# Optimization experiments

Measured on AMD Instinct MI355X. Metric: run time of the kernel, lower is better.

Reference implementation:

```python
import jax, jax.numpy as jnp
import numpy as np

B, T, D_K, N_HEADS, D_FF, VOCAB, N_LAYERS = 4, 1024, 1024, 16, 4096, 65, 6


def setup_inputs() -> dict:
    key = jax.random.key(0)
    ks = jax.random.split(key, 12)
    f = lambda k, sh: jax.random.normal(k, sh, dtype=jnp.float32) * 0.02
    return {
        "batchData": jax.random.randint(ks[0], (B, T), 0, VOCAB),
        "target": jax.random.randint(ks[1], (B, T), 0, VOCAB),
        "pos": jnp.arange(T),
        "Wtok": f(ks[2], (VOCAB, D_K)),
        "Wpos": f(ks[3], (T, D_K)),
        "Wq": f(ks[4], (D_K, D_K)), "bq": jnp.zeros((D_K,), jnp.float32),
        "Wk": f(ks[5], (D_K, D_K)), "bk": jnp.zeros((D_K,), jnp.float32),
        "Wv": f(ks[6], (D_K, D_K)), "bv": jnp.zeros((D_K,), jnp.float32),
        "W1": f(ks[7], (D_K, D_FF)), "b1": jnp.zeros((D_FF,), jnp.float32),
        "W2": f(ks[8], (D_FF, D_K)), "b2": jnp.zeros((D_K,), jnp.float32),
        "ln_w": jnp.ones((D_K,), jnp.float32),
        "Wf": f(ks[9], (D_K, VOCAB)), "bf": jnp.zeros((VOCAB,), jnp.float32),
        "n_layers": N_LAYERS,
        "n_heads": N_HEADS,
    }


def layer_norm(x, w, eps=1e-5):
    m = jnp.mean(x, axis=-1, keepdims=True)
    v = jnp.var(x, axis=-1, keepdims=True)
    return (x - m) / jnp.sqrt(v + eps) * w


def reference(batchData, target, pos, Wtok, Wpos, Wq, bq, Wk, bk, Wv, bv,
              W1, b1, W2, b2, ln_w, Wf, bf, n_layers, n_heads):
    x = Wtok[batchData] + Wpos[pos]  # [B, T, C] (pos embedding broadcasts)
    Bsz, Tlen, C = x.shape
    dh = C // n_heads
    mask = jnp.tril(jnp.ones((Tlen, Tlen), dtype=bool))
    inv_sqrt_dk = 1.0 / jnp.sqrt(jnp.float32(C))  # source divides by sqrt(full d_k)

    def block(x):
        q = (x @ Wq + bq).reshape(Bsz, Tlen, n_heads, dh).transpose(0, 2, 1, 3)
        k = (x @ Wk + bk).reshape(Bsz, Tlen, n_heads, dh).transpose(0, 2, 1, 3)
        v = (x @ Wv + bv).reshape(Bsz, Tlen, n_heads, dh).transpose(0, 2, 1, 3)
        scores = jnp.einsum('bhqd,bhkd->bhqk', q, k) * inv_sqrt_dk
        scores = jnp.where(mask, scores, -jnp.inf)
        attn = jax.nn.softmax(scores, axis=-1)
        h = jnp.einsum('bhqk,bhkd->bhqd', attn, v)
        h = h.transpose(0, 2, 1, 3).reshape(Bsz, Tlen, C)
        h = h + layer_norm(h, ln_w)           # x = x + ln(x) (shared ln)
        ff = jax.nn.relu(h @ W1 + b1) @ W2 + b2
        return ff + layer_norm(ff, ln_w)      # same shared ln again

    # ModuleList repeats the SAME block object, so weights are shared across layers
    for _ in range(n_layers):
        x = block(x)

    logits = x @ Wf + bf                       # [B, T, V]
    probs = jax.nn.softmax(logits, axis=1)     # softmax over T, as in source
    pred = probs.reshape(Bsz * Tlen, -1)
    onehot = jax.nn.one_hot(target.reshape(-1), VOCAB, dtype=jnp.float32)
    # F.cross_entropy with soft (one-hot float) targets
    loss = -jnp.mean(jnp.sum(onehot * jax.nn.log_softmax(pred, axis=-1), axis=-1))
    return loss, probs
```

## Files before the change

kernel.cpp:

```cpp
#include <hip/hip_runtime.h>

typedef __attribute__((ext_vector_type(8))) short bh8;
typedef __attribute__((ext_vector_type(4))) float f4v;

constexpr int VOC = 65;
constexpr int NL  = 6;
constexpr int Mrow = 4096;

__device__ inline float b2f(unsigned short u) {
  union { unsigned int i; float f; } x; x.i = ((unsigned int)u) << 16; return x.f;
}
__device__ inline unsigned short f2b(float f) {
  union { float f; unsigned int i; } x; x.f = f;
  return (unsigned short)((x.i + 0x7FFFu + ((x.i >> 16) & 1u)) >> 16);
}
__device__ inline void gld16(const void* g, void* l) {
  __builtin_amdgcn_global_load_lds(
      (const __attribute__((address_space(1))) unsigned int*)g,
      (__attribute__((address_space(3))) unsigned int*)l, 16, 0, 0);
}
__device__ inline bh8 lds_swz(const unsigned short* base, int row, int colbyte) {
  int off = row * 128 + (colbyte ^ ((row & 7) << 4));
  return *(const bh8*)((const char*)base + off);
}
__device__ inline f4v mfma16(bh8 a, bh8 b, f4v c) {
  return __builtin_amdgcn_mfma_f32_16x16x32_bf16(a, b, c, 0, 0, 0);
}
#define WAITV(n) asm volatile("s_waitcnt vmcnt(" #n ")" ::: "memory")
#define LGKM0 asm volatile("s_waitcnt lgkmcnt(0)" ::: "memory")
#define LGKM8 asm volatile("s_waitcnt lgkmcnt(8)" ::: "memory")
#define SBAR0 __builtin_amdgcn_sched_barrier(0)
#define BAR __builtin_amdgcn_s_barrier()

__global__ __launch_bounds__(256) void wt_conv(const float* __restrict__ src,
    unsigned short* __restrict__ dst, int K, int N) {
  __shared__ float t[32][33];
  int k0 = blockIdx.x * 32, n0 = blockIdx.y * 32;
  int tid = threadIdx.x;
#pragma unroll
  for (int i = 0; i < 4; ++i) {
    int idx = tid + i * 256;
    int kr = idx >> 5, nc = idx & 31;
    t[kr][nc] = (n0 + nc < N) ? src[(size_t)(k0 + kr) * N + n0 + nc] : 0.f;
  }
  __syncthreads();
#pragma unroll
  for (int i = 0; i < 4; ++i) {
    int idx = tid + i * 256;
    int nr = idx >> 5, kc = idx & 31;
    dst[(size_t)(n0 + nr) * K + k0 + kc] = f2b(t[kc][nr]);
  }
}

__global__ __launch_bounds__(256) void bias_prep(
    const float* __restrict__ bq, const float* __restrict__ bk,
    const float* __restrict__ bv, const float* __restrict__ bf,
    float* __restrict__ bqkv, float* __restrict__ bfp) {
  int i = blockIdx.x * 256 + threadIdx.x;
  if (i < 1024) bqkv[i] = bq[i];
  else if (i < 2048) bqkv[i] = bk[i - 1024];
  else if (i < 3072) bqkv[i] = bv[i - 2048];
  else if (i < 3200) bfp[i - 3072] = (i - 3072 < VOC) ? bf[i - 3072] : 0.f;
}

__global__ __launch_bounds__(256) void embed_bf(const int* __restrict__ tok,
    const float* __restrict__ Wtok, const float* __restrict__ Wpos,
    unsigned short* __restrict__ Xb) {
  int bt = blockIdx.x, t = bt & 1023, tid = threadIdx.x;
  int id = tok[bt];
  float4 a = ((const float4*)(Wtok + (size_t)id * 1024))[tid];
  float4 p = ((const float4*)(Wpos + (size_t)t * 1024))[tid];
  ushort4 o;
  o.x = f2b(a.x + p.x); o.y = f2b(a.y + p.y);
  o.z = f2b(a.z + p.z); o.w = f2b(a.w + p.w);
  ((ushort4*)(Xb + (size_t)bt * 1024))[tid] = o;
}

template <bool RELU, bool PART, bool VT>
__global__ __launch_bounds__(512, 1) void gemm256(
    const unsigned short* __restrict__ A, const unsigned short* __restrict__ Bt,
    const float* __restrict__ bias, void* __restrict__ Cout,
    unsigned short* __restrict__ Vtout, long N, long Kloop, long lda, long ldb,
    int MT, int NT, int CM, int CN) {
  __shared__ unsigned short Abuf[2][256 * 64];
  __shared__ unsigned short Bbuf[2][256 * 64];
  const int tid = threadIdx.x, lane = tid & 63, w = tid >> 6;
  const int wr = w >> 2, wc = w & 3;
  const int lr = lane & 15, lh = lane >> 4, lh4 = lh * 4;

  const int x = (int)blockIdx.x & 7, j = (int)blockIdx.x >> 3;
  const int gM = MT / CM;
  const int rowT = (x % gM) * CM + (j % CM);
  const int c = (x / gM) * CN + (j / CM);
  const int colT = c % NT, ksl = c / NT;
  const long row0 = (long)rowT * 256, col0 = (long)colT * 256;
  const long kOff = (long)ksl * Kloop;

  f4v acc[8][4];
#pragma unroll
  for (int i = 0; i < 8; ++i)
#pragma unroll
    for (int jj = 0; jj < 4; ++jj) acc[i][jj] = f4v{0.f, 0.f, 0.f, 0.f};

  const int rg = tid >> 3, sIdx = tid & 7;
  const int ch = sIdx ^ (rg & 7);
  const unsigned short* Ap = A + (row0 + rg) * lda + kOff + ch * 8;
  const unsigned short* Bp = Bt + (col0 + rg) * ldb + kOff + ch * 8;

  auto stA = [&](int t, int h) {
    const long k0 = (long)t << 6;
#pragma unroll
    for (int i = 0; i < 2; ++i)
      gld16(Ap + (long)(h * 128 + i * 64) * lda + k0,
            &Abuf[t & 1][(h * 128 + i * 64) * 64 + tid * 8]);
  };
  auto stB = [&](int t, int h) {
    const long k0 = (long)t << 6;
#pragma unroll
    for (int i = 0; i < 2; ++i)
      gld16(Bp + (long)(h * 128 + i * 64) * ldb + k0,
            &Bbuf[t & 1][(h * 128 + i * 64) * 64 + tid * 8]);
  };

  const int nt = (int)(Kloop >> 6);
  stA(0, 0); stA(0, 1); stB(0, 0); stB(0, 1);
  stA(1, 0); stA(1, 1); stB(1, 0);
  WAITV(6);
  BAR;

  const int sl0 = (lh ^ (lr & 7)) * 8;
  const int sl1 = ((4 + lh) ^ (lr & 7)) * 8;

  for (int t = 0; t < nt; ++t) {
    const unsigned short* Ab = Abuf[t & 1];
    const unsigned short* Bb = Bbuf[t & 1];
    bh8 a0[4][2], a1[4][2], b0[2][2], b1[2][2];
#pragma unroll
    for (int mi = 0; mi < 4; ++mi) {
      const int row = (2 * mi + wr) * 16 + lr;
      a0[mi][0] = *(const bh8*)&Ab[row * 64 + sl0];
      a0[mi][1] = *(const bh8*)&Ab[row * 64 + sl1];
    }
#pragma unroll
    for (int ni = 0; ni < 2; ++ni) {
      const int row = (4 * ni + wc) * 16 + lr;
      b0[ni][0] = *(const bh8*)&Bb[row * 64 + sl0];
      b0[ni][1] = *(const bh8*)&Bb[row * 64 + sl1];
    }
    if (t + 1 < nt) stB(t + 1, 1);
    LGKM8;
    BAR;
    LGKM0; SBAR0;
    __builtin_amdgcn_s_setprio(1);
#pragma unroll
    for (int mi = 0; mi < 4; ++mi)
#pragma unroll
      for (int ni = 0; ni < 2; ++ni) {
        acc[mi][ni] = mfma16(a0[mi][0], b0[ni][0], acc[mi][ni]);
        acc[mi][ni] = mfma16(a0[mi][1], b0[ni][1], acc[mi][ni]);
      }
    __builtin_amdgcn_s_setprio(0);
    BAR;
#pragma unroll
    for (int mi = 0; mi < 4; ++mi) {
      const int row = (2 * (mi + 4) + wr) * 16 + lr;
      a1[mi][0] = *(const bh8*)&Ab[row * 64 + sl0];
      a1[mi][1] = *(const bh8*)&Ab[row * 64 + sl1];
    }
    if (t + 2 < nt) stA(t + 2, 0);
    BAR;
    LGKM0; SBAR0;
    __builtin_amdgcn_s_setprio(1);
#pragma unroll
    for (int mi = 0; mi < 4; ++mi)
#pragma unroll
      for (int ni = 0; ni < 2; ++ni) {
        acc[mi + 4][ni] = mfma16(a1[mi][0], b0[ni][0], acc[mi + 4][ni]);
        acc[mi + 4][ni] = mfma16(a1[mi][1], b0[ni][1], acc[mi + 4][ni]);
      }
    __builtin_amdgcn_s_setprio(0);
    BAR;
#pragma unroll
    for (int ni = 0; ni < 2; ++ni) {
      const int row = (4 * (ni + 2) + wc) * 16 + lr;
      b1[ni][0] = *(const bh8*)&Bb[row * 64 + sl0];
      b1[ni][1] = *(const bh8*)&Bb[row * 64 + sl1];
    }
    if (t + 2 < nt) stA(t + 2, 1);
    BAR;
    LGKM0; SBAR0;
    __builtin_amdgcn_s_setprio(1);
#pragma unroll
    for (int mi = 0; mi < 4; ++mi)
#pragma unroll
      for (int ni = 0; ni < 2; ++ni) {
        acc[mi][ni + 2] = mfma16(a0[mi][0], b1[ni][0], acc[mi][ni + 2]);
        acc[mi][ni + 2] = mfma16(a0[mi][1], b1[ni][1], acc[mi][ni + 2]);
      }
    __builtin_amdgcn_s_setprio(0);
    BAR;
    if (t + 2 < nt) stB(t + 2, 0);
    BAR;
    SBAR0;
    __builtin_amdgcn_s_setprio(1);
#pragma unroll
    for (int mi = 0; mi < 4; ++mi)
#pragma unroll
      for (int ni = 0; ni < 2; ++ni) {
        acc[mi + 4][ni + 2] = mfma16(a1[mi][0], b1[ni][0], acc[mi + 4][ni + 2]);
        acc[mi + 4][ni + 2] = mfma16(a1[mi][1], b1[ni][1], acc[mi + 4][ni + 2]);
      }
    __builtin_amdgcn_s_setprio(0);
    if (t + 1 < nt) {
      if (t + 2 < nt) { WAITV(6); } else { WAITV(0); }
      BAR;
    }
  }

  if (PART) {
    unsigned short* P = (unsigned short*)Cout + (size_t)ksl * 4096 * 1024;
#pragma unroll
    for (int mi = 0; mi < 8; ++mi)
#pragma unroll
      for (int ni = 0; ni < 4; ++ni) {
        long col = col0 + (4 * ni + wc) * 16 + lr;
#pragma unroll
        for (int r = 0; r < 4; ++r) {
          long row = row0 + (2 * mi + wr) * 16 + lh4 + r;
          P[row * N + col] = f2b(acc[mi][ni][r]);
        }
      }
    return;
  }
  if (VT && col0 >= 2048) {
#pragma unroll
    for (int mi = 0; mi < 8; ++mi)
#pragma unroll
      for (int ni = 0; ni < 4; ++ni) {
        int col = (int)col0 + (4 * ni + wc) * 16 + lr;
        float bb = bias[col];
        int cc = col - 2048;
        long row = row0 + (2 * mi + wr) * 16 + lh4;
        int bi = (int)(row >> 10), tt = (int)(row & 1023);
        ushort4 o;
        o.x = f2b(acc[mi][ni][0] + bb);
        o.y = f2b(acc[mi][ni][1] + bb);
        o.z = f2b(acc[mi][ni][2] + bb);
        o.w = f2b(acc[mi][ni][3] + bb);
        *(ushort4*)&Vtout[((size_t)(bi * 16 + (cc >> 6)) * 64 + (cc & 63)) *
                              1024 + tt] = o;
      }
    return;
  }
#pragma unroll
  for (int mi = 0; mi < 8; ++mi)
#pragma unroll
    for (int ni = 0; ni < 4; ++ni) {
      long col = col0 + (4 * ni + wc) * 16 + lr;
      float bb = bias[col];
      const float qsc = (VT && col < 1024) ? 0.03125f : 1.0f;
#pragma unroll
      for (int r = 0; r < 4; ++r) {
        long row = row0 + (2 * mi + wr) * 16 + lh4 + r;
        float v = acc[mi][ni][r] + bb;
        if (VT) v *= qsc;
        if (RELU) v = fmaxf(v, 0.f);
        ((unsigned short*)Cout)[row * N + col] = f2b(v);
      }
    }
}

template <int TM, int TN, bool RELU, bool F32OUT>
__global__ __launch_bounds__(256) void gemm4(
    const unsigned short* __restrict__ A, const unsigned short* __restrict__ Bt,
    const float* __restrict__ bias, void* __restrict__ Cout, long N, long K) {
  constexpr int MI = TM / 32, NI = TN / 32;
  constexpr int ABUF = TM * 64, BBUF = TN * 64;
  __shared__ unsigned short As[2 * ABUF];
  __shared__ unsigned short Bs[2 * BBUF];
  const int tid = threadIdx.x;
  const int lane = tid & 63, w = tid >> 6;
  const int wr = w >> 1, wc = w & 1;
  const int lr = lane & 15, lh = lane >> 4, lh4 = lh * 4;
  const long row0 = (long)blockIdx.x * TM, col0 = (long)blockIdx.y * TN;
  f4v acc[MI][NI];
#pragma unroll
  for (int i = 0; i < MI; ++i)
#pragma unroll
    for (int j = 0; j < NI; ++j) acc[i][j] = f4v{0.f, 0.f, 0.f, 0.f};
  const int rg = tid >> 3, s = tid & 7;
  const int ch = s ^ (rg & 7);
  const unsigned short* Ap = A + (row0 + rg) * K + ch * 8;
  const unsigned short* Bp = Bt + (col0 + rg) * K + ch * 8;
  auto stage = [&](int t, int buf) {
    const long k0 = (long)t << 6;
#pragma unroll
    for (int i = 0; i < MI; ++i)
      gld16(Ap + i * 32 * K + k0, &As[buf * ABUF + (i * 256 + tid) * 8]);
#pragma unroll
    for (int i = 0; i < NI; ++i)
      gld16(Bp + i * 32 * K + k0, &Bs[buf * BBUF + (i * 256 + tid) * 8]);
  };
  const int nt = (int)(K >> 6);
  stage(0, 0);
  for (int t = 0; t < nt; ++t) {
    const int cur = t & 1;
    if (t + 1 < nt) {
      stage(t + 1, cur ^ 1);
      WAITV(6);
    } else {
      WAITV(0);
    }
    BAR;
    const unsigned short* Ab = &As[cur * ABUF];
    const unsigned short* Bb = &Bs[cur * BBUF];
#pragma unroll
    for (int ks = 0; ks < 2; ++ks) {
      bh8 a[MI], b[NI];
      const int slot = ((ks << 2) | lh) ^ (lr & 7);
#pragma unroll
      for (int mi = 0; mi < MI; ++mi) {
        int m = wr * (TM / 2) + mi * 16 + lr;
        a[mi] = *(const bh8*)((const char*)Ab + m * 128 + slot * 16);
      }
#pragma unroll
      for (int ni = 0; ni < NI; ++ni) {
        int n = wc * (TN / 2) + ni * 16 + lr;
        b[ni] = *(const bh8*)((const char*)Bb + n * 128 + slot * 16);
      }
#pragma unroll
      for (int mi = 0; mi < MI; ++mi)
#pragma unroll
        for (int ni = 0; ni < NI; ++ni)
          acc[mi][ni] = mfma16(a[mi], b[ni], acc[mi][ni]);
    }
    BAR;
  }
#pragma unroll
  for (int mi = 0; mi < MI; ++mi) {
#pragma unroll
    for (int ni = 0; ni < NI; ++ni) {
      long col = col0 + wc * (TN / 2) + ni * 16 + lr;
      float bb = bias[col];
#pragma unroll
      for (int r = 0; r < 4; ++r) {
        long row = row0 + wr * (TM / 2) + mi * 16 + lh4 + r;
        float v = acc[mi][ni][r] + bb;
        if (RELU) v = fmaxf(v, 0.f);
        if (F32OUT) ((float*)Cout)[row * N + col] = v;
        else ((unsigned short*)Cout)[row * N + col] = f2b(v);
      }
    }
  }
}

__global__ __launch_bounds__(256) void attn_mfma(
    const unsigned short* __restrict__ QKV, const unsigned short* __restrict__ Vt,
    unsigned short* __restrict__ Hout) {
  __shared__ unsigned short Ks[2][64 * 64];
  __shared__ unsigned short Vs[2][64 * 64];
  __shared__ unsigned short Ps[4][16 * 64];
  const int tid = threadIdx.x, w = tid >> 6, lane = tid & 63;
  const int wid = ((int)blockIdx.x & 7) * 128 + ((int)blockIdx.x >> 3);
  const int bh = wid >> 4;
  const int qt = 15 - (wid & 15);
  const int b = bh >> 4, h = bh & 15;
  const int lr = lane & 15, lh = lane >> 4, lh4 = lh * 4;

  const unsigned short* qp =
      QKV + (size_t)(b * 1024 + qt * 64 + w * 16 + lr) * 3072 + h * 64 + lh * 8;
  bh8 aq0 = *(const bh8*)qp;
  bh8 aq1 = *(const bh8*)(qp + 32);

  f4v o[4];
#pragma unroll
  for (int i = 0; i < 4; ++i) o[i] = f4v{0.f, 0.f, 0.f, 0.f};
  float m = -1e30f, l = 0.f;

  const int r8 = tid >> 3, slot = tid & 7;
  unsigned short* pw = &Ps[w][0];

  auto stage = [&](int kt, int buf) {
    int r = r8, c8 = (slot ^ (r & 7)) * 8;
    gld16(QKV + (size_t)(b * 1024 + kt * 64 + r) * 3072 + 1024 + h * 64 + c8,
          &Ks[buf][tid * 8]);
    gld16(Vt + (size_t)(bh * 64 + r) * 1024 + kt * 64 + c8, &Vs[buf][tid * 8]);
    r = r8 + 32; c8 = (slot ^ (r & 7)) * 8;
    gld16(QKV + (size_t)(b * 1024 + kt * 64 + r) * 3072 + 1024 + h * 64 + c8,
          &Ks[buf][2048 + tid * 8]);
    gld16(Vt + (size_t)(bh * 64 + r) * 1024 + kt * 64 + c8,
          &Vs[buf][2048 + tid * 8]);
  };

  stage(0, 0);

  for (int kt = 0; kt <= qt; ++kt) {
    const int cur = kt & 1;
    if (kt < qt) {
      stage(kt + 1, cur ^ 1);
      WAITV(4);
    } else {
      WAITV(0);
    }
    BAR;

    f4v s[4];
#pragma unroll
    for (int nt = 0; nt < 4; ++nt) {
      bh8 k0 = lds_swz(Ks[cur], nt * 16 + lr, lh * 16);
      bh8 k1 = lds_swz(Ks[cur], nt * 16 + lr, lh * 16 + 64);
      f4v z = f4v{0.f, 0.f, 0.f, 0.f};
      z = mfma16(k0, aq0, z);
      z = mfma16(k1, aq1, z);
      s[nt] = z;
    }
    const bool diag = (kt == qt);
    if (diag) {
      const int qloc = w * 16 + lr;
#pragma unroll
      for (int nt = 0; nt < 4; ++nt)
#pragma unroll
        for (int r = 0; r < 4; ++r)
          if ((nt * 16 + lh4 + r) > qloc) s[nt][r] = -1e30f;
    }
    float tm = fmaxf(fmaxf(fmaxf(s[0][0], s[0][1]), fmaxf(s[0][2], s[0][3])),
                     fmaxf(fmaxf(s[1][0], s[1][1]), fmaxf(s[1][2], s[1][3])));
    float tm2 = fmaxf(fmaxf(fmaxf(s[2][0], s[2][1]), fmaxf(s[2][2], s[2][3])),
                      fmaxf(fmaxf(s[3][0], s[3][1]), fmaxf(s[3][2], s[3][3])));
    tm = fmaxf(tm, tm2);
    tm = fmaxf(tm, __shfl_xor(tm, 16));
    tm = fmaxf(tm, __shfl_xor(tm, 32));

    const bool resc = __any(tm > m + 8.f);
    const float mu = resc ? fmaxf(m, tm) : m;
    float sum = 0.f;
#pragma unroll
    for (int nt = 0; nt < 4; ++nt)
#pragma unroll
      for (int r = 0; r < 4; ++r) {
        float e = __expf(s[nt][r] - mu);
        s[nt][r] = e;
        sum += e;
      }
    sum += __shfl_xor(sum, 16);
    sum += __shfl_xor(sum, 32);
    if (resc) {
      float corr = __expf(m - mu);
      m = mu;
      l = l * corr + sum;
      float c0 = __shfl(corr, lh4 + 0), c1 = __shfl(corr, lh4 + 1);
      float c2 = __shfl(corr, lh4 + 2), c3 = __shfl(corr, lh4 + 3);
#pragma unroll
      for (int nt = 0; nt < 4; ++nt) {
        o[nt][0] *= c0; o[nt][1] *= c1; o[nt][2] *= c2; o[nt][3] *= c3;
      }
    } else {
      l += sum;
    }
#pragma unroll
    for (int nt = 0; nt < 4; ++nt) {
      unsigned int u0, u1;
      asm("v_cvt_pk_bf16_f32 %0, %1, %2" : "=v"(u0) : "v"(s[nt][0]), "v"(s[nt][1]));
      asm("v_cvt_pk_bf16_f32 %0, %1, %2" : "=v"(u1) : "v"(s[nt][2]), "v"(s[nt][3]));
      uint2 pk{u0, u1};
      *(uint2*)((char*)pw + lr * 128 + ((nt * 32 + lh * 8) ^ ((lr & 7) << 4))) = pk;
    }
    bh8 pa0 = lds_swz(pw, lr, lh * 16);
    bh8 pa1 = lds_swz(pw, lr, lh * 16 + 64);
#pragma unroll
    for (int nt = 0; nt < 4; ++nt) {
      bh8 v0 = lds_swz(Vs[cur], nt * 16 + lr, lh * 16);
      bh8 v1 = lds_swz(Vs[cur], nt * 16 + lr, lh * 16 + 64);
      o[nt] = mfma16(pa0, v0, o[nt]);
      o[nt] = mfma16(pa1, v1, o[nt]);
    }
    BAR;
  }
  float linv = 1.f / l;
  float l0 = __shfl(linv, lh4 + 0), l1 = __shfl(linv, lh4 + 1);
  float l2 = __shfl(linv, lh4 + 2), l3 = __shfl(linv, lh4 + 3);
  const size_t rowb = (size_t)(b * 1024 + qt * 64 + w * 16);
#pragma unroll
  for (int nt = 0; nt < 4; ++nt) {
    int col = h * 64 + nt * 16 + lr;
    Hout[(rowb + lh4 + 0) * 1024 + col] = f2b(o[nt][0] * l0);
    Hout[(rowb + lh4 + 1) * 1024 + col] = f2b(o[nt][1] * l1);
    Hout[(rowb + lh4 + 2) * 1024 + col] = f2b(o[nt][2] * l2);
    Hout[(rowb + lh4 + 3) * 1024 + col] = f2b(o[nt][3] * l3);
  }
}

__global__ __launch_bounds__(256) void ln_res_bf(
    const unsigned short* __restrict__ Xi, const float* __restrict__ wln,
    unsigned short* __restrict__ Y) {
  int row = blockIdx.x, tid = threadIdx.x;
  ushort4 u = ((const ushort4*)(Xi + (size_t)row * 1024))[tid];
  float x0 = b2f(u.x), x1 = b2f(u.y), x2 = b2f(u.z), x3 = b2f(u.w);
  float s = x0 + x1 + x2 + x3;
  float ss = x0 * x0 + x1 * x1 + x2 * x2 + x3 * x3;
#pragma unroll
  for (int off = 32; off; off >>= 1) {
    s += __shfl_xor(s, off);
    ss += __shfl_xor(ss, off);
  }
  __shared__ float sw[4], ssw[4];
  int wv = tid >> 6, ln = tid & 63;
  if (ln == 0) { sw[wv] = s; ssw[wv] = ss; }
  __syncthreads();
  s = sw[0] + sw[1] + sw[2] + sw[3];
  ss = ssw[0] + ssw[1] + ssw[2] + ssw[3];
  float mean = s * (1.f / 1024.f);
  float var = ss * (1.f / 1024.f) - mean * mean;
  float rstd = rsqrtf(var + 1e-5f);
  float4 wv4 = ((const float4*)wln)[tid];
  ushort4 out;
  out.x = f2b(x0 + (x0 - mean) * rstd * wv4.x);
  out.y = f2b(x1 + (x1 - mean) * rstd * wv4.y);
  out.z = f2b(x2 + (x2 - mean) * rstd * wv4.z);
  out.w = f2b(x3 + (x3 - mean) * rstd * wv4.w);
  ((ushort4*)(Y + (size_t)row * 1024))[tid] = out;
}

__global__ __launch_bounds__(256) void ln2_fuse(
    const unsigned short* __restrict__ P, const float* __restrict__ b2,
    const float* __restrict__ wln, unsigned short* __restrict__ Y) {
  int row = blockIdx.x, tid = threadIdx.x;
  const size_t plane = (size_t)4096 * 1024;
  float x0 = 0.f, x1 = 0.f, x2 = 0.f, x3 = 0.f;
#pragma unroll
  for (int pl = 0; pl < 4; ++pl) {
    ushort4 u = *(const ushort4*)&P[pl * plane + (size_t)row * 1024 + tid * 4];
    x0 += b2f(u.x); x1 += b2f(u.y); x2 += b2f(u.z); x3 += b2f(u.w);
  }
  float4 bb = ((const float4*)b2)[tid];
  x0 += bb.x; x1 += bb.y; x2 += bb.z; x3 += bb.w;
  float s = x0 + x1 + x2 + x3;
  float ss = x0 * x0 + x1 * x1 + x2 * x2 + x3 * x3;
#pragma unroll
  for (int off = 32; off; off >>= 1) {
    s += __shfl_xor(s, off);
    ss += __shfl_xor(ss, off);
  }
  __shared__ float sw[4], ssw[4];
  int wv = tid >> 6, ln = tid & 63;
  if (ln == 0) { sw[wv] = s; ssw[wv] = ss; }
  __syncthreads();
  s = sw[0] + sw[1] + sw[2] + sw[3];
  ss = ssw[0] + ssw[1] + ssw[2] + ssw[3];
  float mean = s * (1.f / 1024.f);
  float var = ss * (1.f / 1024.f) - mean * mean;
  float rstd = rsqrtf(var + 1e-5f);
  float4 wv4 = ((const float4*)wln)[tid];
  ushort4 out;
  out.x = f2b(x0 + (x0 - mean) * rstd * wv4.x);
  out.y = f2b(x1 + (x1 - mean) * rstd * wv4.y);
  out.z = f2b(x2 + (x2 - mean) * rstd * wv4.z);
  out.w = f2b(x3 + (x3 - mean) * rstd * wv4.w);
  ((ushort4*)(Y + (size_t)row * 1024))[tid] = out;
}

__global__ __launch_bounds__(256) void softmaxT_kernel(
    const float* __restrict__ logits, float* __restrict__ probs) {
  int b = blockIdx.x / VOC;
  int v = blockIdx.x - b * VOC;
  const float* src = logits + (size_t)b * 1024 * 128 + v;
  float vals[4];
  float m = -1e30f;
#pragma unroll
  for (int i = 0; i < 4; ++i) {
    int t = threadIdx.x + 256 * i;
    vals[i] = src[(size_t)t * 128];
    m = fmaxf(m, vals[i]);
  }
#pragma unroll
  for (int off = 32; off; off >>= 1) m = fmaxf(m, __shfl_xor(m, off));
  __shared__ float sm[4], ssum[4];
  int wv = threadIdx.x >> 6, ln = threadIdx.x & 63;
  if (ln == 0) sm[wv] = m;
  __syncthreads();
  m = fmaxf(fmaxf(sm[0], sm[1]), fmaxf(sm[2], sm[3]));
  float s = 0.f;
#pragma unroll
  for (int i = 0; i < 4; ++i) { vals[i] = __expf(vals[i] - m); s += vals[i]; }
#pragma unroll
  for (int off = 32; off; off >>= 1) s += __shfl_xor(s, off);
  if (ln == 0) ssum[wv] = s;
  __syncthreads();
  s = ssum[0] + ssum[1] + ssum[2] + ssum[3];
  float inv = 1.f / s;
  float* dst = probs + (size_t)b * 1024 * VOC + v;
#pragma unroll
  for (int i = 0; i < 4; ++i) {
    int t = threadIdx.x + 256 * i;
    dst[(size_t)t * VOC] = vals[i] * inv;
  }
}

__global__ __launch_bounds__(256) void loss_rows_kernel(
    const float* __restrict__ probs, const int* __restrict__ tgt,
    float* __restrict__ partial) {
  int wv = threadIdx.x >> 6, lane = threadIdx.x & 63;
  int row = blockIdx.x * 4 + wv;
  const float* p = probs + (size_t)row * VOC;
  float x0 = p[lane];
  float x1 = (lane == 0) ? p[64] : -1e30f;
  float m = fmaxf(x0, x1);
#pragma unroll
  for (int off = 32; off; off >>= 1) m = fmaxf(m, __shfl_xor(m, off));
  float s = __expf(x0 - m) + ((lane == 0) ? __expf(x1 - m) : 0.f);
#pragma unroll
  for (int off = 32; off; off >>= 1) s += __shfl_xor(s, off);
  if (lane == 0) {
    int tg = tgt[row];
    partial[row] = (p[tg] - m) - logf(s);
  }
}

__global__ __launch_bounds__(256) void loss_final_kernel(
    const float* __restrict__ partial, float* __restrict__ out) {
  float s = 0.f;
  for (int i = threadIdx.x; i < Mrow; i += 256) s += partial[i];
#pragma unroll
  for (int off = 32; off; off >>= 1) s += __shfl_xor(s, off);
  __shared__ float sw[4];
  int wv = threadIdx.x >> 6, ln = threadIdx.x & 63;
  if (ln == 0) sw[wv] = s;
  __syncthreads();
  if (threadIdx.x == 0) out[0] = -(sw[0] + sw[1] + sw[2] + sw[3]) / (float)Mrow;
}

extern "C" void kernel_launch(void* const* d_in, const int* in_sizes, int n_in,
                              void* d_out, int out_size, void* d_ws,
                              size_t ws_size, hipStream_t stream) {
  (void)in_sizes; (void)n_in; (void)out_size; (void)ws_size;
  const int*   tok    = (const int*)d_in[0];
  const int*   target = (const int*)d_in[1];
  const float* Wtok   = (const float*)d_in[3];
  const float* Wpos   = (const float*)d_in[4];
  const float* Wq = (const float*)d_in[5];  const float* bq = (const float*)d_in[6];
  const float* Wk = (const float*)d_in[7];  const float* bk = (const float*)d_in[8];
  const float* Wv = (const float*)d_in[9];  const float* bv = (const float*)d_in[10];
  const float* W1 = (const float*)d_in[11]; const float* b1 = (const float*)d_in[12];
  const float* W2 = (const float*)d_in[13]; const float* b2 = (const float*)d_in[14];
  const float* lnw = (const float*)d_in[15];
  const float* Wf = (const float*)d_in[16]; const float* bf = (const float*)d_in[17];
  float* out = (float*)d_out;

  char* p = (char*)d_ws;
  unsigned short* Xb    = (unsigned short*)p; p += (size_t)Mrow * 1024 * 2;
  unsigned short* QKVb  = (unsigned short*)p; p += (size_t)Mrow * 3072 * 2;
  unsigned short* Vt    = (unsigned short*)p; p += (size_t)64 * 64 * 1024 * 2;
  unsigned short* Hb    = (unsigned short*)p; p += (size_t)Mrow * 1024 * 2;
  unsigned short* F2b   = (unsigned short*)p; p += (size_t)Mrow * 1024 * 2;
  unsigned short* FF1b  = (unsigned short*)p; p += (size_t)Mrow * 4096 * 2;
  unsigned short* WqkvT = (unsigned short*)p; p += (size_t)3072 * 1024 * 2;
  unsigned short* W1T   = (unsigned short*)p; p += (size_t)4096 * 1024 * 2;
  unsigned short* W2T   = (unsigned short*)p; p += (size_t)1024 * 4096 * 2;
  unsigned short* WfT   = (unsigned short*)p; p += (size_t)128 * 1024 * 2;
  float* bqkv = (float*)p; p += 3072 * 4;
  float* bfp  = (float*)p; p += 128 * 4;
  float* LOG  = (float*)p; p += (size_t)Mrow * 128 * 4;
  float* PART = (float*)p; p += Mrow * 4;
  unsigned short* Pff2 = QKVb;

  wt_conv<<<dim3(32, 32), 256, 0, stream>>>(Wq, WqkvT,                1024, 1024);
  wt_conv<<<dim3(32, 32), 256, 0, stream>>>(Wk, WqkvT + 1024 * 1024,  1024, 1024);
  wt_conv<<<dim3(32, 32), 256, 0, stream>>>(Wv, WqkvT + 2048 * 1024,  1024, 1024);
  wt_conv<<<dim3(32, 128), 256, 0, stream>>>(W1, W1T, 1024, 4096);
  wt_conv<<<dim3(128, 32), 256, 0, stream>>>(W2, W2T, 4096, 1024);
  wt_conv<<<dim3(32, 4), 256, 0, stream>>>(Wf, WfT, 1024, VOC);
  bias_prep<<<13, 256, 0, stream>>>(bq, bk, bv, bf, bqkv, bfp);

  embed_bf<<<Mrow, 256, 0, stream>>>(tok, Wtok, Wpos, Xb);

  for (int l = 0; l < NL; ++l) {
    gemm256<false, false, true><<<192, 512, 0, stream>>>(
        Xb, WqkvT, bqkv, QKVb, Vt, 3072, 1024, 1024, 1024, 16, 12, 4, 6);
    attn_mfma<<<1024, 256, 0, stream>>>(QKVb, Vt, Hb);
    ln_res_bf<<<Mrow, 256, 0, stream>>>(Hb, lnw, F2b);
    gemm256<true, false, false><<<256, 512, 0, stream>>>(
        F2b, W1T, b1, FF1b, nullptr, 4096, 1024, 1024, 1024, 16, 16, 4, 8);
    gemm256<false, true, false><<<256, 512, 0, stream>>>(
        FF1b, W2T, nullptr, Pff2, nullptr, 1024, 1024, 4096, 4096, 16, 4, 4, 8);
    ln2_fuse<<<Mrow, 256, 0, stream>>>(Pff2, b2, lnw, Xb);
  }

  gemm4<64, 128, false, true><<<dim3(64, 1), 256, 0, stream>>>(
      Xb, WfT, bfp, LOG, 128, 1024);
  softmaxT_kernel<<<4 * VOC, 256, 0, stream>>>(LOG, out + 1);
  loss_rows_kernel<<<Mrow / 4, 256, 0, stream>>>(out + 1, target, PART);
  loss_final_kernel<<<1, 256, 0, stream>>>(PART, out);
}
```

Baseline: 994.6 us.

## Run FFN GEMMs in FP8 e4m3 with scaled activations and weights

Converts W1/W2 weights and the FFN input activations to FP8 e4m3 with a fixed x16 scale, and adds a new 256x256 FP8 MFMA GEMM kernel for both FFN matmuls. The first GEMM writes its ReLU output directly in FP8 and the second writes split-K bf16 partials descaled by 1/256. This targets the MFMA throughput and memory traffic of the two largest GEMMs, at the cost of lower numerical precision and possible saturation or underflow with fixed scaling.

```diff
diff --git a/kernel.cpp b/kernel.cpp
--- a/kernel.cpp
+++ b/kernel.cpp
@@ -13,6 +13,14 @@
 __device__ inline unsigned short f2b(float f) {
   union { float f; unsigned int i; } x; x.f = f;
   return (unsigned short)((x.i + 0x7FFFu + ((x.i >> 16) & 1u)) >> 16);
+}
+__device__ inline unsigned char f2e4m3(float v) {
+  return (unsigned char)(__builtin_amdgcn_cvt_pk_fp8_f32(v, v, 0, false) & 0xFF);
+}
+__device__ inline unsigned int pk4_e4m3(float a, float b, float c, float d) {
+  int v = __builtin_amdgcn_cvt_pk_fp8_f32(a, b, 0, false);
+  v = __builtin_amdgcn_cvt_pk_fp8_f32(c, d, v, true);
+  return (unsigned int)v;
 }
 __device__ inline void gld16(const void* g, void* l) {
   __builtin_amdgcn_global_load_lds(
@@ -25,6 +33,9 @@
 }
 __device__ inline f4v mfma16(bh8 a, bh8 b, f4v c) {
   return __builtin_amdgcn_mfma_f32_16x16x32_bf16(a, b, c, 0, 0, 0);
+}
+__device__ inline f4v mfma8(long a, long b, f4v c) {
+  return __builtin_amdgcn_mfma_f32_16x16x32_fp8_fp8(a, b, c, 0, 0, 0);
 }
 #define WAITV(n) asm volatile("s_waitcnt vmcnt(" #n ")" ::: "memory")
 #define LGKM0 asm volatile("s_waitcnt lgkmcnt(0)" ::: "memory")
@@ -49,6 +60,26 @@
     int idx = tid + i * 256;
     int nr = idx >> 5, kc = idx & 31;
     dst[(size_t)(n0 + nr) * K + k0 + kc] = f2b(t[kc][nr]);
+  }
+}
+
+__global__ __launch_bounds__(256) void wt_conv8(const float* __restrict__ src,
+    unsigned char* __restrict__ dst, int K, int N) {
+  __shared__ float t[32][33];
+  int k0 = blockIdx.x * 32, n0 = blockIdx.y * 32;
+  int tid = threadIdx.x;
+#pragma unroll
+  for (int i = 0; i < 4; ++i) {
+    int idx = tid + i * 256;
+    int kr = idx >> 5, nc = idx & 31;
+    t[kr][nc] = (n0 + nc < N) ? src[(size_t)(k0 + kr) * N + n0 + nc] : 0.f;
+  }
+  __syncthreads();
+#pragma unroll
+  for (int i = 0; i < 4; ++i) {
+    int idx = tid + i * 256;
+    int nr = idx >> 5, kc = idx & 31;
+    dst[(size_t)(n0 + nr) * K + k0 + kc] = f2e4m3(t[kc][nr] * 16.f);
   }
 }
 
@@ -266,6 +297,179 @@
         if (VT) v *= qsc;
         if (RELU) v = fmaxf(v, 0.f);
         ((unsigned short*)Cout)[row * N + col] = f2b(v);
+      }
+    }
+}
+
+template <bool PART>
+__global__ __launch_bounds__(512, 1) void gemm256f8(
+    const unsigned char* __restrict__ A, const unsigned char* __restrict__ Bt,
+    const float* __restrict__ bias, void* __restrict__ Cout,
+    long N, long Kloop, long lda, long ldb, int MT, int NT, int CM, int CN) {
+  __shared__ unsigned char Abuf[2][256 * 128];
+  __shared__ unsigned char Bbuf[2][256 * 128];
+  const int tid = threadIdx.x, lane = tid & 63, w = tid >> 6;
+  const int wr = w >> 2, wc = w & 3;
+  const int lr = lane & 15, lh = lane >> 4, lh4 = lh * 4;
+
+  const int x = (int)blockIdx.x & 7, j = (int)blockIdx.x >> 3;
+  const int gM = MT / CM;
+  const int rowT = (x % gM) * CM + (j % CM);
+  const int c = (x / gM) * CN + (j / CM);
+  const int colT = c % NT, ksl = c / NT;
+  const long row0 = (long)rowT * 256, col0 = (long)colT * 256;
+  const long kOff = (long)ksl * Kloop;
+
+  f4v acc[8][4];
+#pragma unroll
+  for (int i = 0; i < 8; ++i)
+#pragma unroll
+    for (int jj = 0; jj < 4; ++jj) acc[i][jj] = f4v{0.f, 0.f, 0.f, 0.f};
+
+  const int rg = tid >> 3, sIdx = tid & 7;
+  const int ch = sIdx ^ (rg & 7);
+  const unsigned char* Ap = A + (row0 + rg) * lda + kOff + ch * 16;
+  const unsigned char* Bp = Bt + (col0 + rg) * ldb + kOff + ch * 16;
+
+  auto stA = [&](int t, int h) {
+    const long k0 = (long)t << 7;
+#pragma unroll
+    for (int i = 0; i < 2; ++i)
+      gld16(Ap + (long)(h * 128 + i * 64) * lda + k0,
+            &Abuf[t & 1][(h * 128 + i * 64) * 128 + tid * 16]);
+  };
+  auto stB = [&](int t, int h) {
+    const long k0 = (long)t << 7;
+#pragma unroll
+    for (int i = 0; i < 2; ++i)
+      gld16(Bp + (long)(h * 128 + i * 64) * ldb + k0,
+            &Bbuf[t & 1][(h * 128 + i * 64) * 128 + tid * 16]);
+  };
+
+  const int nt = (int)(Kloop >> 7);
+  stA(0, 0); stA(0, 1); stB(0, 0); stB(0, 1);
+  stA(1, 0); stA(1, 1); stB(1, 0);
+  WAITV(6);
+  BAR;
+
+  int fsl[4];
+#pragma unroll
+  for (int ks = 0; ks < 4; ++ks)
+    fsl[ks] = (((ks * 2 + (lh >> 1)) ^ (lr & 7)) << 4) + (lh & 1) * 8;
+
+  for (int t = 0; t < nt; ++t) {
+    const unsigned char* Ab = Abuf[t & 1];
+    const unsigned char* Bb = Bbuf[t & 1];
+    long a0[4][4], a1[4][4], b0[2][4], b1[2][4];
+#pragma unroll
+    for (int mi = 0; mi < 4; ++mi) {
+      const unsigned char* rp = &Ab[((2 * mi + wr) * 16 + lr) * 128];
+#pragma unroll
+      for (int ks = 0; ks < 4; ++ks) a0[mi][ks] = *(const long*)&rp[fsl[ks]];
+    }
+#pragma unroll
+    for (int ni = 0; ni < 2; ++ni) {
+      const unsigned char* rp = &Bb[((4 * ni + wc) * 16 + lr) * 128];
+#pragma unroll
+      for (int ks = 0; ks < 4; ++ks) b0[ni][ks] = *(const long*)&rp[fsl[ks]];
+    }
+    if (t + 1 < nt) stB(t + 1, 1);
+    LGKM8;
+    BAR;
+    LGKM0; SBAR0;
+    __builtin_amdgcn_s_setprio(1);
+#pragma unroll
+    for (int ks = 0; ks < 4; ++ks)
+#pragma unroll
+      for (int mi = 0; mi < 4; ++mi)
+#pragma unroll
+        for (int ni = 0; ni < 2; ++ni)
+          acc[mi][ni] = mfma8(a0[mi][ks], b0[ni][ks], acc[mi][ni]);
+    __builtin_amdgcn_s_setprio(0);
+    BAR;
+#pragma unroll
+    for (int mi = 0; mi < 4; ++mi) {
+      const unsigned char* rp = &Ab[((2 * (mi + 4) + wr) * 16 + lr) * 128];
+#pragma unroll
+      for (int ks = 0; ks < 4; ++ks) a1[mi][ks] = *(const long*)&rp[fsl[ks]];
+    }
+    if (t + 2 < nt) stA(t + 2, 0);
+    BAR;
+    LGKM0; SBAR0;
+    __builtin_amdgcn_s_setprio(1);
+#pragma unroll
+    for (int ks = 0; ks < 4; ++ks)
+#pragma unroll
+      for (int mi = 0; mi < 4; ++mi)
+#pragma unroll
+        for (int ni = 0; ni < 2; ++ni)
+          acc[mi + 4][ni] = mfma8(a1[mi][ks], b0[ni][ks], acc[mi + 4][ni]);
+    __builtin_amdgcn_s_setprio(0);
+    BAR;
+#pragma unroll
+    for (int ni = 0; ni < 2; ++ni) {
+      const unsigned char* rp = &Bb[((4 * (ni + 2) + wc) * 16 + lr) * 128];
+#pragma unroll
+      for (int ks = 0; ks < 4; ++ks) b1[ni][ks] = *(const long*)&rp[fsl[ks]];
+    }
+    if (t + 2 < nt) stA(t + 2, 1);
+    BAR;
+    LGKM0; SBAR0;
+    __builtin_amdgcn_s_setprio(1);
+#pragma unroll
+    for (int ks = 0; ks < 4; ++ks)
+#pragma unroll
+      for (int mi = 0; mi < 4; ++mi)
+#pragma unroll
+        for (int ni = 0; ni < 2; ++ni)
+          acc[mi][ni + 2] = mfma8(a0[mi][ks], b1[ni][ks], acc[mi][ni + 2]);
+    __builtin_amdgcn_s_setprio(0);
+    BAR;
+    if (t + 2 < nt) stB(t + 2, 0);
+    BAR;
+    SBAR0;
+    __builtin_amdgcn_s_setprio(1);
+#pragma unroll
+    for (int ks = 0; ks < 4; ++ks)
+#pragma unroll
+      for (int mi = 0; mi < 4; ++mi)
+#pragma unroll
+        for (int ni = 0; ni < 2; ++ni)
+          acc[mi + 4][ni + 2] = mfma8(a1[mi][ks], b1[ni][ks], acc[mi + 4][ni + 2]);
+    __builtin_amdgcn_s_setprio(0);
+    if (t + 1 < nt) {
+      if (t + 2 < nt) { WAITV(6); } else { WAITV(0); }
+      BAR;
+    }
+  }
+
+  constexpr float DS = 1.f / 256.f;
+  if (PART) {
+    unsigned short* P = (unsigned short*)Cout + (size_t)ksl * 4096 * 1024;
+#pragma unroll
+    for (int mi = 0; mi < 8; ++mi)
+#pragma unroll
+      for (int ni = 0; ni < 4; ++ni) {
+        long col = col0 + (4 * ni + wc) * 16 + lr;
+#pragma unroll
+        for (int r = 0; r < 4; ++r) {
+          long row = row0 + (2 * mi + wr) * 16 + lh4 + r;
+          P[row * N + col] = f2b(acc[mi][ni][r] * DS);
+        }
+      }
+    return;
+  }
+#pragma unroll
+  for (int mi = 0; mi < 8; ++mi)
+#pragma unroll
+    for (int ni = 0; ni < 4; ++ni) {
+      long col = col0 + (4 * ni + wc) * 16 + lr;
+      float bb = bias[col];
+#pragma unroll
+      for (int r = 0; r < 4; ++r) {
+        long row = row0 + (2 * mi + wr) * 16 + lh4 + r;
+        float v = fmaxf(acc[mi][ni][r] * DS + bb, 0.f);
+        ((unsigned char*)Cout)[row * N + col] = f2e4m3(v * 16.f);
       }
     }
 }
@@ -490,12 +694,57 @@
   }
 }
 
+template <bool FP8>
 __global__ __launch_bounds__(256) void ln_res_bf(
     const unsigned short* __restrict__ Xi, const float* __restrict__ wln,
-    unsigned short* __restrict__ Y) {
+    void* __restrict__ Y) {
   int row = blockIdx.x, tid = threadIdx.x;
   ushort4 u = ((const ushort4*)(Xi + (size_t)row * 1024))[tid];
   float x0 = b2f(u.x), x1 = b2f(u.y), x2 = b2f(u.z), x3 = b2f(u.w);
+  float s = x0 + x1 + x2 + x3;
+  float ss = x0 * x0 + x1 * x1 + x2 * x2 + x3 * x3;
+#pragma unroll
+  for (int off = 32; off; off >>= 1) {
+    s += __shfl_xor(s, off);
+    ss += __shfl_xor(ss, off);
+  }
+  __shared__ float sw[4], ssw[4];
+  int wv = tid >> 6, ln = tid & 63;
+  if (ln == 0) { sw[wv] = s; ssw[wv] = ss; }
+  __syncthreads();
+  s = sw[0] + sw[1] + sw[2] + sw[3];
+  ss = ssw[0] + ssw[1] + ssw[2] + ssw[3];
+  float mean = s * (1.f / 1024.f);
+  float var = ss * (1.f / 1024.f) - mean * mean;
+  float rstd = rsqrtf(var + 1e-5f);
+  float4 wv4 = ((const float4*)wln)[tid];
+  float y0 = x0 + (x0 - mean) * rstd * wv4.x;
+  float y1 = x1 + (x1 - mean) * rstd * wv4.y;
+  float y2 = x2 + (x2 - mean) * rstd * wv4.z;
+  float y3 = x3 + (x3 - mean) * rstd * wv4.w;
+  if (FP8) {
+    ((unsigned int*)Y)[row * 256 + tid] =
+        pk4_e4m3(y0 * 16.f, y1 * 16.f, y2 * 16.f, y3 * 16.f);
+  } else {
+    ushort4 out;
+    out.x = f2b(y0); out.y = f2b(y1); out.z = f2b(y2); out.w = f2b(y3);
+    ((ushort4*)Y)[row * 256 + tid] = out;
+  }
+}
+
+__global__ __launch_bounds__(256) void ln2_fuse(
+    const unsigned short* __restrict__ P, const float* __restrict__ b2,
+    const float* __restrict__ wln, unsigned short* __restrict__ Y) {
+  int row = blockIdx.x, tid = threadIdx.x;
+  const size_t plane = (size_t)4096 * 1024;
+  float x0 = 0.f, x1 = 0.f, x2 = 0.f, x3 = 0.f;
+#pragma unroll
+  for (int pl = 0; pl < 4; ++pl) {
+    ushort4 u = *(const ushort4*)&P[pl * plane + (size_t)row * 1024 + tid * 4];
+    x0 += b2f(u.x); x1 += b2f(u.y); x2 += b2f(u.z); x3 += b2f(u.w);
+  }
+  float4 bb = ((const float4*)b2)[tid];
+  x0 += bb.x; x1 += bb.y; x2 += bb.z; x3 += bb.w;
   float s = x0 + x1 + x2 + x3;
   float ss = x0 * x0 + x1 * x1 + x2 * x2 + x3 * x3;
 #pragma unroll
@@ -521,44 +770,6 @@
   ((ushort4*)(Y + (size_t)row * 1024))[tid] = out;
 }
 
-__global__ __launch_bounds__(256) void ln2_fuse(
-    const unsigned short* __restrict__ P, const float* __restrict__ b2,
-    const float* __restrict__ wln, unsigned short* __restrict__ Y) {
-  int row = blockIdx.x, tid = threadIdx.x;
-  const size_t plane = (size_t)4096 * 1024;
-  float x0 = 0.f, x1 = 0.f, x2 = 0.f, x3 = 0.f;
-#pragma unroll
-  for (int pl = 0; pl < 4; ++pl) {
-    ushort4 u = *(const ushort4*)&P[pl * plane + (size_t)row * 1024 + tid * 4];
-    x0 += b2f(u.x); x1 += b2f(u.y); x2 += b2f(u.z); x3 += b2f(u.w);
-  }
-  float4 bb = ((const float4*)b2)[tid];
-  x0 += bb.x; x1 += bb.y; x2 += bb.z; x3 += bb.w;
-  float s = x0 + x1 + x2 + x3;
-  float ss = x0 * x0 + x1 * x1 + x2 * x2 + x3 * x3;
-#pragma unroll
-  for (int off = 32; off; off >>= 1) {
-    s += __shfl_xor(s, off);
-    ss += __shfl_xor(ss, off);
-  }
-  __shared__ float sw[4], ssw[4];
-  int wv = tid >> 6, ln = tid & 63;
-  if (ln == 0) { sw[wv] = s; ssw[wv] = ss; }
-  __syncthreads();
-  s = sw[0] + sw[1] + sw[2] + sw[3];
-  ss = ssw[0] + ssw[1] + ssw[2] + ssw[3];
-  float mean = s * (1.f / 1024.f);
-  float var = ss * (1.f / 1024.f) - mean * mean;
-  float rstd = rsqrtf(var + 1e-5f);
-  float4 wv4 = ((const float4*)wln)[tid];
-  ushort4 out;
-  out.x = f2b(x0 + (x0 - mean) * rstd * wv4.x);
-  out.y = f2b(x1 + (x1 - mean) * rstd * wv4.y);
-  out.z = f2b(x2 + (x2 - mean) * rstd * wv4.z);
-  out.w = f2b(x3 + (x3 - mean) * rstd * wv4.w);
-  ((ushort4*)(Y + (size_t)row * 1024))[tid] = out;
-}
-
 __global__ __launch_bounds__(256) void softmaxT_kernel(
     const float* __restrict__ logits, float* __restrict__ probs) {
   int b = blockIdx.x / VOC;
@@ -651,11 +862,11 @@
   unsigned short* QKVb  = (unsigned short*)p; p += (size_t)Mrow * 3072 * 2;
   unsigned short* Vt    = (unsigned short*)p; p += (size_t)64 * 64 * 1024 * 2;
   unsigned short* Hb    = (unsigned short*)p; p += (size_t)Mrow * 1024 * 2;
-  unsigned short* F2b   = (unsigned short*)p; p += (size_t)Mrow * 1024 * 2;
-  unsigned short* FF1b  = (unsigned short*)p; p += (size_t)Mrow * 4096 * 2;
+  unsigned char*  F2b8  = (unsigned char*)p;  p += (size_t)Mrow * 1024 * 2;
+  unsigned char*  FF1b8 = (unsigned char*)p;  p += (size_t)Mrow * 4096 * 2;
   unsigned short* WqkvT = (unsigned short*)p; p += (size_t)3072 * 1024 * 2;
-  unsigned short* W1T   = (unsigned short*)p; p += (size_t)4096 * 1024 * 2;
-  unsigned short* W2T   = (unsigned short*)p; p += (size_t)1024 * 4096 * 2;
+  unsigned char*  W1T8  = (unsigned char*)p;  p += (size_t)4096 * 1024 * 2;
+  unsigned char*  W2T8  = (unsigned char*)p;  p += (size_t)1024 * 4096 * 2;
   unsigned short* WfT   = (unsigned short*)p; p += (size_t)128 * 1024 * 2;
   float* bqkv = (float*)p; p += 3072 * 4;
   float* bfp  = (float*)p; p += 128 * 4;
@@ -666,8 +877,8 @@
   wt_conv<<<dim3(32, 32), 256, 0, stream>>>(Wq, WqkvT,                1024, 1024);
   wt_conv<<<dim3(32, 32), 256, 0, stream>>>(Wk, WqkvT + 1024 * 1024,  1024, 1024);
   wt_conv<<<dim3(32, 32), 256, 0, stream>>>(Wv, WqkvT + 2048 * 1024,  1024, 1024);
-  wt_conv<<<dim3(32, 128), 256, 0, stream>>>(W1, W1T, 1024, 4096);
-  wt_conv<<<dim3(128, 32), 256, 0, stream>>>(W2, W2T, 4096, 1024);
+  wt_conv8<<<dim3(32, 128), 256, 0, stream>>>(W1, W1T8, 1024, 4096);
+  wt_conv8<<<dim3(128, 32), 256, 0, stream>>>(W2, W2T8, 4096, 1024);
   wt_conv<<<dim3(32, 4), 256, 0, stream>>>(Wf, WfT, 1024, VOC);
   bias_prep<<<13, 256, 0, stream>>>(bq, bk, bv, bf, bqkv, bfp);
 
@@ -677,11 +888,11 @@
     gemm256<false, false, true><<<192, 512, 0, stream>>>(
         Xb, WqkvT, bqkv, QKVb, Vt, 3072, 1024, 1024, 1024, 16, 12, 4, 6);
     attn_mfma<<<1024, 256, 0, stream>>>(QKVb, Vt, Hb);
-    ln_res_bf<<<Mrow, 256, 0, stream>>>(Hb, lnw, F2b);
-    gemm256<true, false, false><<<256, 512, 0, stream>>>(
-        F2b, W1T, b1, FF1b, nullptr, 4096, 1024, 1024, 1024, 16, 16, 4, 8);
-    gemm256<false, true, false><<<256, 512, 0, stream>>>(
-        FF1b, W2T, nullptr, Pff2, nullptr, 1024, 1024, 4096, 4096, 16, 4, 4, 8);
+    ln_res_bf<true><<<Mrow, 256, 0, stream>>>(Hb, lnw, F2b8);
+    gemm256f8<false><<<256, 512, 0, stream>>>(
+        F2b8, W1T8, b1, FF1b8, 4096, 1024, 1024, 1024, 16, 16, 4, 8);
+    gemm256f8<true><<<256, 512, 0, stream>>>(
+        FF1b8, W2T8, nullptr, Pff2, 1024, 1024, 4096, 4096, 16, 4, 4, 8);
     ln2_fuse<<<Mrow, 256, 0, stream>>>(Pff2, b2, lnw, Xb);
   }
 
```

After: 1.001 ms. No clear change (+0.7%).
